# Kernel tuning notes

Measured on AMD Instinct MI355X. Metric: run time of the kernel, lower is better.

The kernel has to match this reference:

```python
import jax, jax.numpy as jnp
import numpy as np

TEMP = 0.5   # temperature from __init__
EPS = 1e-8   # torch.nn.CosineSimilarity eps


def setup_inputs() -> dict:
    key = jax.random.key(0)
    N, D = 8192, 256
    x = jax.random.normal(key, (N, D), dtype=jnp.float32)
    # pairs: each label appears exactly twice, as required for the
    # sim[~mask].reshape(N, -1) in the original to be well-formed
    y = jnp.arange(N, dtype=jnp.int32) // 2
    return {"x": x, "y": y}


def reference(x, y):
    # cosine similarity matrix: normalize once, then one NxD @ DxN matmul
    # (equivalent to CosineSimilarity(x.unsqueeze(1), x.unsqueeze(0)) without
    #  the NxNxD intermediate)
    norm = jnp.maximum(jnp.linalg.norm(x, axis=1, keepdims=True), EPS)
    xn = x / norm
    sim = (xn @ xn.T) / TEMP                     # [N, N]

    # Original: positives = equal-label entries (row-major order, includes the
    # diagonal), logits = [positives | negatives] which is just a per-row
    # permutation of sim; labels = 0 -> CE target is the FIRST equal-label
    # column of each row. logsumexp is over the full row (all N entries).
    eq = y[:, None] == y[None, :]                # [N, N] bool
    first_pos = jnp.argmax(eq, axis=1)           # first column j with y_j == y_i
    target = jnp.take_along_axis(sim, first_pos[:, None], axis=1)[:, 0]  # [N]

    lse = jax.nn.logsumexp(sim, axis=1)          # [N]
    N = x.shape[0]
    loss = jnp.sum(lse - target) / N             # CrossEntropyLoss(sum) / N
    return loss
```

## Files before the change

kernel.cpp:

```cpp
#include <hip/hip_runtime.h>
#include <hip/hip_bf16.h>

#define D 256
#define INV_TEMP 2.0f

typedef __attribute__((ext_vector_type(8))) short short8;
typedef __attribute__((ext_vector_type(4))) float floatx4;

__device__ __forceinline__ unsigned short f2bf(float f) {
    union { float f; unsigned u; } a; a.f = f;
    unsigned r = (a.u + 0x7fffu + ((a.u >> 16) & 1u)) >> 16;
    return (unsigned short)r;
}

__device__ __forceinline__ void gload_lds16(const unsigned short* g,
                                            unsigned short* l) {
    __builtin_amdgcn_global_load_lds(
        (const __attribute__((address_space(1))) unsigned int*)g,
        (__attribute__((address_space(3))) unsigned int*)l, 16, 0, 0);
}

__global__ void nt_prep_kernel(const float* __restrict__ x,
                               unsigned short* __restrict__ xnb,
                               float* __restrict__ pair_dot) {
    int p    = blockIdx.x * 4 + (threadIdx.x >> 6);
    int lane = threadIdx.x & 63;
    const float4* a4 = (const float4*)(x + (size_t)(2 * p) * D);
    const float4* b4 = (const float4*)(x + (size_t)(2 * p + 1) * D);
    float4 a = a4[lane], b = b4[lane];
    float saa = a.x * a.x + a.y * a.y + a.z * a.z + a.w * a.w;
    float sbb = b.x * b.x + b.y * b.y + b.z * b.z + b.w * b.w;
    float sab = a.x * b.x + a.y * b.y + a.z * b.z + a.w * b.w;
    #pragma unroll
    for (int off = 32; off; off >>= 1) {
        saa += __shfl_xor(saa, off);
        sbb += __shfl_xor(sbb, off);
        sab += __shfl_xor(sab, off);
    }
    float inva = 1.0f / fmaxf(sqrtf(saa), 1e-8f);
    float invb = 1.0f / fmaxf(sqrtf(sbb), 1e-8f);
    ushort4 oa, ob;
    oa.x = f2bf(a.x * inva); oa.y = f2bf(a.y * inva);
    oa.z = f2bf(a.z * inva); oa.w = f2bf(a.w * inva);
    ob.x = f2bf(b.x * invb); ob.y = f2bf(b.y * invb);
    ob.z = f2bf(b.z * invb); ob.w = f2bf(b.w * invb);
    ((ushort4*)(xnb + (size_t)(2 * p) * D))[lane] = oa;
    ((ushort4*)(xnb + (size_t)(2 * p + 1) * D))[lane] = ob;
    if (lane == 0)
        pair_dot[p] = sab * inva * invb * INV_TEMP;
}

__global__ __launch_bounds__(256, 2)
void nt_simexp_kernel(const unsigned short* __restrict__ xnb,
                      float* __restrict__ contrib) {
    __shared__ __align__(16) unsigned short Bs[128 * 256];

    const int p  = blockIdx.x >> 4, q = blockIdx.x & 15;
    const int s1 = 63 - p;
    const int c0 = 64 - p;
    const int q0 = (p + q) & 15;

    const int tid  = threadIdx.x;
    const int wave = tid >> 6, lane = tid & 63;
    const int wm   = wave & 1, wn = wave >> 1;
    const int quad = lane >> 4, c = lane & 15;

    auto strip_of = [&](int i) { return (i < c0) ? p : s1; };
    auto bi_of    = [&](int i) { return (i < c0) ? (p + i) : (s1 + i - c0); };

    auto load_B = [&](int bj) {
        const unsigned short* src = xnb + (size_t)(bj * 128) * D;
        int rs = lane >> 5, pp = lane & 31;
        #pragma unroll
        for (int t = 0; t < 16; ++t) {
            int wl = wave * 16 + t;
            int rr = wl * 2 + rs;
            int j  = (pp & ~7) | ((pp ^ rr) & 7);
            gload_lds16(src + (size_t)rr * D + j * 8, Bs + wl * 512 + lane * 8);
        }
    };

    auto load_A = [&](int bi, int h, short8 af[4][2]) {
        const unsigned short* src =
            xnb + (size_t)(bi * 128 + wm * 64 + c) * D + h * 64 + quad * 8;
        #pragma unroll
        for (int mt = 0; mt < 4; ++mt)
            #pragma unroll
            for (int ks = 0; ks < 2; ++ks)
                af[mt][ks] = *(const short8*)(src + (size_t)(mt * 16) * D + ks * 32);
    };

    floatx4 acc[4][4];
    auto compute = [&](short8 af[4][2], int h) {
        #pragma unroll
        for (int ks = 0; ks < 2; ++ks) {
            const int jg = h * 8 + ks * 4 + quad;
            const int pB = (jg & ~7) | ((jg ^ c) & 7);
            short8 bf[4];
            #pragma unroll
            for (int nt = 0; nt < 4; ++nt)
                bf[nt] = *(const short8*)(Bs + (wn * 64 + nt * 16 + c) * 256 + pB * 8);
            #pragma unroll
            for (int mt = 0; mt < 4; ++mt)
                #pragma unroll
                for (int nt = 0; nt < 4; ++nt)
                    acc[mt][nt] = __builtin_amdgcn_mfma_f32_16x16x32_bf16(
                        af[mt][ks], bf[nt], acc[mt][nt], 0, 0, 0);
        }
    };

    short8 afb[2][4][2];
    int bj = strip_of(q0);
    load_B(bj);
    load_A(bi_of(q0), 0, afb[0]);
    __syncthreads();

    for (int i = q0; i < 65; i += 16) {
        const int bi = bi_of(i);
        const int ni = i + 16;
        const bool have_next = (ni < 65);
        const int nbj = have_next ? strip_of(ni) : -1;

        #pragma unroll
        for (int mt = 0; mt < 4; ++mt)
            #pragma unroll
            for (int nt = 0; nt < 4; ++nt)
                acc[mt][nt] = (floatx4){0.f, 0.f, 0.f, 0.f};

        #pragma unroll
        for (int h = 0; h < 4; ++h) {
            if (h < 3)            load_A(bi, h + 1, afb[(h + 1) & 1]);
            else if (have_next)   load_A(bi_of(ni), 0, afb[0]);
            compute(afb[h & 1], h);
        }

        #pragma unroll
        for (int mt = 0; mt < 4; ++mt)
            #pragma unroll
            for (int nt = 0; nt < 4; ++nt)
                #pragma unroll
                for (int r = 0; r < 4; ++r)
                    acc[mt][nt][r] = __expf(acc[mt][nt][r] * INV_TEMP);

        #pragma unroll
        for (int mt = 0; mt < 4; ++mt) {
            float ps[4] = {0.f, 0.f, 0.f, 0.f};
            #pragma unroll
            for (int nt = 0; nt < 4; ++nt)
                #pragma unroll
                for (int r = 0; r < 4; ++r)
                    ps[r] += acc[mt][nt][r];
            #pragma unroll
            for (int off = 1; off < 16; off <<= 1)
                #pragma unroll
                for (int r = 0; r < 4; ++r)
                    ps[r] += __shfl_xor(ps[r], off);
            if (c == 0) {
                float4 v = {ps[0], ps[1], ps[2], ps[3]};
                *(float4*)(contrib + (((size_t)bi * 64 + bj) * 2 + wn) * 128 +
                           wm * 64 + mt * 16 + quad * 4) = v;
            }
        }
        if (bi != bj) {
            #pragma unroll
            for (int nt = 0; nt < 4; ++nt) {
                float cs = 0.f;
                #pragma unroll
                for (int mt = 0; mt < 4; ++mt)
                    #pragma unroll
                    for (int r = 0; r < 4; ++r)
                        cs += acc[mt][nt][r];
                cs += __shfl_xor(cs, 16);
                cs += __shfl_xor(cs, 32);
                if (quad == 0)
                    contrib[(((size_t)bj * 64 + bi) * 2 + wm) * 128 +
                            wn * 64 + nt * 16 + c] = cs;
            }
        }

        if (have_next && nbj != bj) {
            __syncthreads();
            load_B(nbj);
            __syncthreads();
            bj = nbj;
        }
    }
}

__global__ void nt_reduce_kernel(const float* __restrict__ contrib,
                                 const float* __restrict__ pair_dot,
                                 float* __restrict__ blockPart) {
    __shared__ float sm[256];
    int b  = blockIdx.x;
    int rl = threadIdx.x & 127, h = threadIdx.x >> 7;
    float s = 0.f;
    const float* base = contrib + (((size_t)b * 64) * 2 + h) * 128 + rl;
    #pragma unroll
    for (int j = 0; j < 64; ++j) s += base[(size_t)j * 256];
    sm[threadIdx.x] = s;
    __syncthreads();
    float v = 0.f;
    if (h == 0) v = logf(sm[rl] + sm[128 + rl]);
    else if (rl < 64) v = -pair_dot[b * 64 + rl];
    __syncthreads();
    sm[threadIdx.x] = v;
    __syncthreads();
    for (int st = 128; st; st >>= 1) {
        if ((int)threadIdx.x < st) sm[threadIdx.x] += sm[threadIdx.x + st];
        __syncthreads();
    }
    if (threadIdx.x == 0) blockPart[b] = sm[0];
}

__global__ void nt_final_kernel(const float* __restrict__ blockPart,
                                float* __restrict__ out, int N) {
    int lane = threadIdx.x & 63;
    float s = blockPart[lane];
    #pragma unroll
    for (int off = 32; off; off >>= 1) s += __shfl_xor(s, off);
    if (lane == 0) out[0] = (s - (float)N) / (float)N;
}

extern "C" void kernel_launch(void* const* d_in, const int* in_sizes, int n_in,
                              void* d_out, int out_size, void* d_ws, size_t ws_size,
                              hipStream_t stream) {
    const float* x = (const float*)d_in[0];
    int N = in_sizes[0] / D;

    char* ws = (char*)d_ws;
    unsigned short* xnb = (unsigned short*)ws;
    float* pair_dot  = (float*)(ws + (size_t)N * D * 2);
    float* contrib   = pair_dot + N / 2;
    float* blockPart = contrib + (size_t)64 * 64 * 2 * 128;

    nt_prep_kernel<<<N / 8, 256, 0, stream>>>(x, xnb, pair_dot);
    nt_simexp_kernel<<<512, 256, 0, stream>>>(xnb, contrib);
    nt_reduce_kernel<<<N / 128, 256, 0, stream>>>(contrib, pair_dot, blockPart);
    nt_final_kernel<<<1, 64, 0, stream>>>(blockPart, (float*)d_out, N);
}
```

Measured before the change: 111.6 us.

## Split symmetric sim tiles into 128x64 strips with masked diagonal and per-strip column sums

Reorganizes the symmetric similarity work from 128x128 tile pairs into 128-row by 64-column strips, assigning each block a pair of complementary column strips. Diagonal-straddling tiles are masked, so each entry's exp is counted once for the row sum and once for the column sum. Column sums are kept in registers across a strip and flushed only when the strip changes. The grid doubles to 1024 blocks, LDS halves, and occupancy rises to 4 blocks per CU. The cost is smaller tiles with less MFMA reuse per A-fragment load, per-element mask branches, and a reduce kernel with a different gather pattern.

```diff
diff --git a/kernel.cpp b/kernel.cpp
--- a/kernel.cpp
+++ b/kernel.cpp
@@ -50,48 +50,45 @@
         pair_dot[p] = sab * inva * invb * INV_TEMP;
 }
 
-__global__ __launch_bounds__(256, 2)
+__global__ __launch_bounds__(256, 4)
 void nt_simexp_kernel(const unsigned short* __restrict__ xnb,
-                      float* __restrict__ contrib) {
-    __shared__ __align__(16) unsigned short Bs[128 * 256];
+                      float* __restrict__ rowC,
+                      float* __restrict__ colC) {
+    __shared__ __align__(16) unsigned short Bs[64 * 256];
 
     const int p  = blockIdx.x >> 4, q = blockIdx.x & 15;
-    const int s1 = 63 - p;
-    const int c0 = 64 - p;
-    const int q0 = (p + q) & 15;
+    const int s0 = p, s1 = 127 - p;
+    const int n0 = 64 - (s0 >> 1);
+    const int r0 = (p + q) & 15;
 
     const int tid  = threadIdx.x;
     const int wave = tid >> 6, lane = tid & 63;
-    const int wm   = wave & 1, wn = wave >> 1;
     const int quad = lane >> 4, c = lane & 15;
 
-    auto strip_of = [&](int i) { return (i < c0) ? p : s1; };
-    auto bi_of    = [&](int i) { return (i < c0) ? (p + i) : (s1 + i - c0); };
-
-    auto load_B = [&](int bj) {
-        const unsigned short* src = xnb + (size_t)(bj * 128) * D;
-        int rs = lane >> 5, pp = lane & 31;
-        #pragma unroll
-        for (int t = 0; t < 16; ++t) {
-            int wl = wave * 16 + t;
-            int rr = wl * 2 + rs;
-            int j  = (pp & ~7) | ((pp ^ rr) & 7);
-            gload_lds16(src + (size_t)rr * D + j * 8, Bs + wl * 512 + lane * 8);
-        }
-    };
-
-    auto load_A = [&](int bi, int h, short8 af[4][2]) {
+    auto load_B = [&](int s) {
+        const unsigned short* src = xnb + (size_t)(s * 64) * D;
+        #pragma unroll
+        for (int t = 0; t < 8; ++t) {
+            int wl = wave * 8 + t;
+            int ci = wl * 64 + lane;
+            int r  = ci >> 5, pos = ci & 31;
+            int j  = (pos & ~7) | ((pos ^ r) & 7);
+            gload_lds16(src + (size_t)r * D + j * 8, Bs + wl * 512 + lane * 8);
+        }
+    };
+
+    auto load_A = [&](int bi, int h, short8 af[2][2]) {
         const unsigned short* src =
-            xnb + (size_t)(bi * 128 + wm * 64 + c) * D + h * 64 + quad * 8;
-        #pragma unroll
-        for (int mt = 0; mt < 4; ++mt)
+            xnb + (size_t)(bi * 128 + wave * 32 + c) * D + h * 64 + quad * 8;
+        #pragma unroll
+        for (int mt = 0; mt < 2; ++mt)
             #pragma unroll
             for (int ks = 0; ks < 2; ++ks)
                 af[mt][ks] = *(const short8*)(src + (size_t)(mt * 16) * D + ks * 32);
     };
 
-    floatx4 acc[4][4];
-    auto compute = [&](short8 af[4][2], int h) {
+    floatx4 acc[2][4];
+    auto compute = [&](short8 af[2][2], int h) {
         #pragma unroll
         for (int ks = 0; ks < 2; ++ks) {
             const int jg = h * 8 + ks * 4 + quad;
@@ -99,9 +96,9 @@
             short8 bf[4];
             #pragma unroll
             for (int nt = 0; nt < 4; ++nt)
-                bf[nt] = *(const short8*)(Bs + (wn * 64 + nt * 16 + c) * 256 + pB * 8);
-            #pragma unroll
-            for (int mt = 0; mt < 4; ++mt)
+                bf[nt] = *(const short8*)(Bs + (nt * 16 + c) * 256 + pB * 8);
+            #pragma unroll
+            for (int mt = 0; mt < 2; ++mt)
                 #pragma unroll
                 for (int nt = 0; nt < 4; ++nt)
                     acc[mt][nt] = __builtin_amdgcn_mfma_f32_16x16x32_bf16(
@@ -109,107 +106,127 @@
         }
     };
 
-    short8 afb[2][4][2];
-    int bj = strip_of(q0);
-    load_B(bj);
-    load_A(bi_of(q0), 0, afb[0]);
+    auto map_u = [&](int u, int& s, int& bi) {
+        if (u < n0) { s = s0; bi = (s0 >> 1) + u; }
+        else        { s = s1; bi = (s1 >> 1) + (u - n0); }
+    };
+
+    float cs[4] = {0.f, 0.f, 0.f, 0.f};
+    auto flush_cs = [&](int s) {
+        #pragma unroll
+        for (int nt = 0; nt < 4; ++nt) {
+            float v = cs[nt];
+            v += __shfl_xor(v, 16);
+            v += __shfl_xor(v, 32);
+            if (quad == 0)
+                colC[(((size_t)s * 16 + q) * 4 + wave) * 64 + nt * 16 + c] = v;
+            cs[nt] = 0.f;
+        }
+    };
+
+    short8 afb[2][2][2];
+    int cur_s, bi0;
+    map_u(r0, cur_s, bi0);
+    load_B(cur_s);
+    load_A(bi0, 0, afb[0]);
     __syncthreads();
 
-    for (int i = q0; i < 65; i += 16) {
-        const int bi = bi_of(i);
-        const int ni = i + 16;
-        const bool have_next = (ni < 65);
-        const int nbj = have_next ? strip_of(ni) : -1;
-
-        #pragma unroll
-        for (int mt = 0; mt < 4; ++mt)
+    for (int u = r0; u < 65; u += 16) {
+        int s, bi; map_u(u, s, bi);
+        const int nu = u + 16;
+        const bool have_next = (nu < 65);
+        int ns = s, nbi = bi;
+        if (have_next) map_u(nu, ns, nbi);
+
+        if (s != cur_s) {
+            flush_cs(cur_s);
+            __syncthreads();
+            load_B(s);
+            __syncthreads();
+            cur_s = s;
+        }
+
+        #pragma unroll
+        for (int mt = 0; mt < 2; ++mt)
             #pragma unroll
             for (int nt = 0; nt < 4; ++nt)
                 acc[mt][nt] = (floatx4){0.f, 0.f, 0.f, 0.f};
 
         #pragma unroll
         for (int h = 0; h < 4; ++h) {
-            if (h < 3)            load_A(bi, h + 1, afb[(h + 1) & 1]);
-            else if (have_next)   load_A(bi_of(ni), 0, afb[0]);
+            if (h < 3)          load_A(bi, h + 1, afb[(h + 1) & 1]);
+            else if (have_next) load_A(nbi, 0, afb[0]);
             compute(afb[h & 1], h);
         }
 
-        #pragma unroll
-        for (int mt = 0; mt < 4; ++mt)
-            #pragma unroll
-            for (int nt = 0; nt < 4; ++nt)
+        const bool straddle = (bi == (s >> 1));
+        #pragma unroll
+        for (int mt = 0; mt < 2; ++mt) {
+            float pr[4] = {0.f, 0.f, 0.f, 0.f};
+            #pragma unroll
+            for (int nt = 0; nt < 4; ++nt) {
+                const int j = s * 64 + nt * 16 + c;
                 #pragma unroll
-                for (int r = 0; r < 4; ++r)
-                    acc[mt][nt][r] = __expf(acc[mt][nt][r] * INV_TEMP);
-
-        #pragma unroll
-        for (int mt = 0; mt < 4; ++mt) {
-            float ps[4] = {0.f, 0.f, 0.f, 0.f};
-            #pragma unroll
-            for (int nt = 0; nt < 4; ++nt)
-                #pragma unroll
-                for (int r = 0; r < 4; ++r)
-                    ps[r] += acc[mt][nt][r];
+                for (int r = 0; r < 4; ++r) {
+                    float e = __expf(acc[mt][nt][r] * INV_TEMP);
+                    if (straddle) {
+                        const int i = bi * 128 + wave * 32 + mt * 16 + quad * 4 + r;
+                        pr[r]  += (j <= i) ? e : 0.f;
+                        cs[nt] += (j <  i) ? e : 0.f;
+                    } else {
+                        pr[r]  += e;
+                        cs[nt] += e;
+                    }
+                }
+            }
             #pragma unroll
             for (int off = 1; off < 16; off <<= 1)
                 #pragma unroll
                 for (int r = 0; r < 4; ++r)
-                    ps[r] += __shfl_xor(ps[r], off);
+                    pr[r] += __shfl_xor(pr[r], off);
             if (c == 0) {
-                float4 v = {ps[0], ps[1], ps[2], ps[3]};
-                *(float4*)(contrib + (((size_t)bi * 64 + bj) * 2 + wn) * 128 +
-                           wm * 64 + mt * 16 + quad * 4) = v;
+                float4 v = {pr[0], pr[1], pr[2], pr[3]};
+                *(float4*)(rowC + ((size_t)bi * 128 + s) * 128 +
+                           wave * 32 + mt * 16 + quad * 4) = v;
             }
         }
-        if (bi != bj) {
-            #pragma unroll
-            for (int nt = 0; nt < 4; ++nt) {
-                float cs = 0.f;
-                #pragma unroll
-                for (int mt = 0; mt < 4; ++mt)
-                    #pragma unroll
-                    for (int r = 0; r < 4; ++r)
-                        cs += acc[mt][nt][r];
-                cs += __shfl_xor(cs, 16);
-                cs += __shfl_xor(cs, 32);
-                if (quad == 0)
-                    contrib[(((size_t)bj * 64 + bi) * 2 + wm) * 128 +
-                            wn * 64 + nt * 16 + c] = cs;
-            }
-        }
-
-        if (have_next && nbj != bj) {
-            __syncthreads();
-            load_B(nbj);
-            __syncthreads();
-            bj = nbj;
-        }
-    }
-}
-
-__global__ void nt_reduce_kernel(const float* __restrict__ contrib,
+    }
+    flush_cs(cur_s);
+    if (cur_s == s0) {
+        if (quad == 0)
+            #pragma unroll
+            for (int nt = 0; nt < 4; ++nt)
+                colC[(((size_t)s1 * 16 + q) * 4 + wave) * 64 + nt * 16 + c] = 0.f;
+    }
+}
+
+__global__ void nt_reduce_kernel(const float* __restrict__ rowC,
+                                 const float* __restrict__ colC,
                                  const float* __restrict__ pair_dot,
                                  float* __restrict__ blockPart) {
     __shared__ float sm[256];
-    int b  = blockIdx.x;
-    int rl = threadIdx.x & 127, h = threadIdx.x >> 7;
-    float s = 0.f;
-    const float* base = contrib + (((size_t)b * 64) * 2 + h) * 128 + rl;
-    #pragma unroll
-    for (int j = 0; j < 64; ++j) s += base[(size_t)j * 256];
-    sm[threadIdx.x] = s;
-    __syncthreads();
+    const int bi = blockIdx.x, t = threadIdx.x;
     float v = 0.f;
-    if (h == 0) v = logf(sm[rl] + sm[128 + rl]);
-    else if (rl < 64) v = -pair_dot[b * 64 + rl];
-    __syncthreads();
-    sm[threadIdx.x] = v;
+    if (t < 128) {
+        float s = 0.f;
+        const float* base = rowC + ((size_t)bi * 128) * 128 + t;
+        const int smax = 2 * bi + 1;
+        for (int ss = 0; ss <= smax; ++ss) s += base[(size_t)ss * 128];
+        const int i = bi * 128 + t, si = i >> 6;
+        const float* cb = colC + ((size_t)si * 16) * 4 * 64 + (i & 63);
+        #pragma unroll
+        for (int k = 0; k < 64; ++k) s += cb[k * 64];
+        v = logf(s);
+    } else if (t < 192) {
+        v = -pair_dot[bi * 64 + (t - 128)];
+    }
+    sm[t] = v;
     __syncthreads();
     for (int st = 128; st; st >>= 1) {
-        if ((int)threadIdx.x < st) sm[threadIdx.x] += sm[threadIdx.x + st];
+        if (t < st) sm[t] += sm[t + st];
         __syncthreads();
     }
-    if (threadIdx.x == 0) blockPart[b] = sm[0];
+    if (t == 0) blockPart[bi] = sm[0];
 }
 
 __global__ void nt_final_kernel(const float* __restrict__ blockPart,
@@ -230,11 +247,12 @@
     char* ws = (char*)d_ws;
     unsigned short* xnb = (unsigned short*)ws;
     float* pair_dot  = (float*)(ws + (size_t)N * D * 2);
-    float* contrib   = pair_dot + N / 2;
-    float* blockPart = contrib + (size_t)64 * 64 * 2 * 128;
+    float* rowC      = pair_dot + N / 2;
+    float* colC      = rowC + (size_t)64 * 128 * 128;
+    float* blockPart = colC + (size_t)128 * 16 * 4 * 64;
 
     nt_prep_kernel<<<N / 8, 256, 0, stream>>>(x, xnb, pair_dot);
-    nt_simexp_kernel<<<512, 256, 0, stream>>>(xnb, contrib);
-    nt_reduce_kernel<<<N / 128, 256, 0, stream>>>(contrib, pair_dot, blockPart);
+    nt_simexp_kernel<<<1024, 256, 0, stream>>>(xnb, rowC, colC);
+    nt_reduce_kernel<<<64, 256, 0, stream>>>(rowC, colC, pair_dot, blockPart);
     nt_final_kernel<<<1, 64, 0, stream>>>(blockPart, (float*)d_out, N);
 }
```

Result: slower. 145.2 us (+30.1%).
